# Optimization experiments

Measured on AMD Instinct MI355X. Metric: run time of the kernel, lower is better.

Reference implementation:

```python
import jax, jax.numpy as jnp
import numpy as np

N = 50000        # num nodes
NFEAT = 512      # input feature dim
NCLASS = 256     # output classes (out_features of out_att)
E_RAND = 800000  # random edges; + N self-loops
NEG_SLOPE = 0.2  # leakyrelu alpha


def setup_inputs() -> dict:
    key = jax.random.key(0)
    k1, k2, k3, k4 = jax.random.split(key, 4)
    x = jax.random.normal(k1, (N, NFEAT), dtype=jnp.float32)
    W = jax.random.normal(k2, (NFEAT, NCLASS), dtype=jnp.float32) / np.float32(np.sqrt(NFEAT))
    a = jax.random.normal(k3, (2 * NCLASS,), dtype=jnp.float32) / np.float32(np.sqrt(2 * NCLASS))
    rand_edges = jax.random.randint(k4, (2, E_RAND), 0, N, dtype=jnp.int32)
    self_loops = jnp.tile(jnp.arange(N, dtype=jnp.int32), (2, 1))
    edge_index = jnp.concatenate([rand_edges, self_loops], axis=1)  # [2, E]
    return {"x": x, "W": W, "a": a, "edge_index": edge_index}


def reference(x, W, a, edge_index):
    # Eval-mode SpGAT: dropout is identity (training=False).
    row, col = edge_index[0], edge_index[1]  # edge = adj.nonzero().t(): row aggregates from col
    h = x @ W                                # [N, F]
    F_out = h.shape[1]
    # a @ cat(h[row], h[col]) == (h @ a1)[row] + (h @ a2)[col]  (avoids [E, 2F] concat)
    s_row = h @ a[:F_out]                    # [N]
    s_col = h @ a[F_out:]                    # [N]
    logits = s_row[row] + s_col[col]         # [E]
    e = jnp.exp(-jax.nn.leaky_relu(logits, negative_slope=NEG_SLOPE))  # [E]
    rowsum = jax.ops.segment_sum(e, row, num_segments=N)               # [N]
    msgs = e[:, None] * h[col]                                         # [E, F]
    h_prime = jax.ops.segment_sum(msgs, row, num_segments=N) / rowsum[:, None]
    return jax.nn.log_softmax(jax.nn.elu(h_prime), axis=1)
```

## Files before the change

### kernel.cpp

```cpp
#include <hip/hip_runtime.h>
#include <math.h>

#define NNODES   50000
#define NFEAT    512
#define NCLASS   256
#define NEG_SLOPE 0.2f
#define MPAD     50048
#define GBLK     782
#define BCAP     64

typedef __attribute__((ext_vector_type(8))) short short8;
typedef __attribute__((ext_vector_type(4))) float floatx4;

__device__ __forceinline__ unsigned short f2bf(float f) {
    unsigned u = __builtin_bit_cast(unsigned, f);
    u += 0x7fffu + ((u >> 16) & 1u);
    return (unsigned short)(u >> 16);
}
__device__ __forceinline__ float bf2f_lo(unsigned u) {
    return __builtin_bit_cast(float, u << 16);
}
__device__ __forceinline__ float bf2f_hi(unsigned u) {
    return __builtin_bit_cast(float, u & 0xffff0000u);
}
__device__ __forceinline__ unsigned pack_bf16_rh(float lo, float hi) {
    const unsigned ulo = __builtin_bit_cast(unsigned, lo) + 0x8000u;
    const unsigned uhi = __builtin_bit_cast(unsigned, hi) + 0x8000u;
    return __builtin_amdgcn_perm(uhi, ulo, 0x07060302);
}

#if __has_builtin(__builtin_amdgcn_fdot2_f32_bf16)
#define HAVE_DOT2 1
typedef __attribute__((ext_vector_type(2))) __bf16 bfx2;
__device__ __forceinline__ float dot2bf(unsigned hpair, unsigned epair, float acc) {
    return __builtin_amdgcn_fdot2_f32_bf16(__builtin_bit_cast(bfx2, hpair),
                                           __builtin_bit_cast(bfx2, epair), acc, false);
}
#endif

__global__ __launch_bounds__(256) void init_kernel(const float* __restrict__ W,
                                                   unsigned short* __restrict__ Wt,
                                                   int* __restrict__ cursor, int zn) {
    const int i = blockIdx.x * 256 + threadIdx.x;
    const int n = i >> 9;
    const int k = i & 511;
    Wt[i] = f2bf(W[(size_t)k * NCLASS + n]);
    if (i < zn) cursor[i] = 0;
}

__global__ __launch_bounds__(256, 4) void gemm_mfma_kernel(const float* __restrict__ x,
                                                           const unsigned short* __restrict__ Wt,
                                                           unsigned short* __restrict__ hb,
                                                           const float* __restrict__ a,
                                                           float* __restrict__ s_row,
                                                           float* __restrict__ s_col,
                                                           int M) {
    __shared__ union {
        struct { short As[2][64 * 32]; short Bs[2][256 * 32]; } k;
        short Cs[32 * 260];
    } u;

    const int tid  = threadIdx.x;
    const int w    = tid >> 6;
    const int lane = tid & 63;
    const int rowbase = blockIdx.x * 64;

    const int wm = w & 1;
    const int wn = w >> 1;
    const int srow = lane >> 2;
    const int skq  = (lane & 3) << 3;
    const int fm = lane & 15;
    const int fq = lane >> 4;

    floatx4 acc[2][8];
#pragma unroll
    for (int i = 0; i < 2; ++i)
#pragma unroll
        for (int j = 0; j < 8; ++j)
            acc[i][j] = (floatx4){0.f, 0.f, 0.f, 0.f};

    const int arow = min(rowbase + w * 16 + srow, M - 1);
    const size_t abase = (size_t)arow * NFEAT + skq;
    const int lrowA = (w * 16 + srow) * 32 + skq;

#define STAGE_B(buf, k0)                                                                      \
    {                                                                                         \
        _Pragma("unroll")                                                                     \
        for (int t = 0; t < 4; ++t) {                                                         \
            const int seg = w * 4 + t;                                                        \
            const int nr  = seg * 16 + srow;                                                  \
            __builtin_amdgcn_global_load_lds(                                                 \
                (const __attribute__((address_space(1))) void*)(Wt + (size_t)nr * NFEAT + (k0) + skq), \
                (__attribute__((address_space(3))) void*)(&u.k.Bs[buf][seg * 512]), 16, 0, 0); \
        }                                                                                     \
    }

    STAGE_B(0, 0)
    {
        const float4* xp = (const float4*)&x[abase];
        const float4 u0 = xp[0];
        const float4 u1 = xp[1];
        uint4 o;
        o.x = pack_bf16_rh(u0.x, u0.y);
        o.y = pack_bf16_rh(u0.z, u0.w);
        o.z = pack_bf16_rh(u1.x, u1.y);
        o.w = pack_bf16_rh(u1.z, u1.w);
        *(uint4*)&u.k.As[0][lrowA] = o;
    }
    __syncthreads();

    int cur = 0;
    for (int k0 = 0; k0 < NFEAT; k0 += 32) {
        const int nxt = cur ^ 1;
        const bool have_next = (k0 + 32) < NFEAT;
        float4 p0, p1;
        if (have_next) {
            const float4* xp = (const float4*)&x[abase + k0 + 32];
            p0 = xp[0];
            p1 = xp[1];
            STAGE_B(nxt, k0 + 32)
        }

        short8 af[2];
#pragma unroll
        for (int mt = 0; mt < 2; ++mt)
            af[mt] = *(const short8*)&u.k.As[cur][(wm * 32 + mt * 16 + fm) * 32 + fq * 8];
#pragma unroll
        for (int nt = 0; nt < 8; ++nt) {
            const short8 bfr = *(const short8*)&u.k.Bs[cur][(wn * 128 + nt * 16 + fm) * 32 + fq * 8];
#pragma unroll
            for (int mt = 0; mt < 2; ++mt)
                acc[mt][nt] = __builtin_amdgcn_mfma_f32_16x16x32_bf16(af[mt], bfr, acc[mt][nt], 0, 0, 0);
        }

        if (have_next) {
            uint4 o;
            o.x = pack_bf16_rh(p0.x, p0.y);
            o.y = pack_bf16_rh(p0.z, p0.w);
            o.z = pack_bf16_rh(p1.x, p1.y);
            o.w = pack_bf16_rh(p1.z, p1.w);
            *(uint4*)&u.k.As[nxt][lrowA] = o;
        }
        __syncthreads();
        cur = nxt;
    }

#pragma unroll
    for (int p = 0; p < 2; ++p) {
        __syncthreads();
        if (wm == p) {
#pragma unroll
            for (int mt = 0; mt < 2; ++mt)
#pragma unroll
                for (int nt = 0; nt < 8; ++nt)
#pragma unroll
                    for (int r = 0; r < 4; ++r)
                        u.Cs[(mt * 16 + fq * 4 + r) * 260 + wn * 128 + nt * 16 + fm] =
                            (short)f2bf(acc[mt][nt][r]);
        }
        __syncthreads();
#pragma unroll
        for (int k = 0; k < 8; ++k) {
            const int idx = tid + k * 256;
            const int lrow = idx >> 6;
            const int c4 = (idx & 63) << 2;
            const int grow = rowbase + p * 32 + lrow;
            const uint2 vv = *(const uint2*)&u.Cs[lrow * 260 + c4];
            const float f0 = bf2f_lo(vv.x), f1 = bf2f_hi(vv.x);
            const float f2 = bf2f_lo(vv.y), f3 = bf2f_hi(vv.y);
            const float4 A1 = *(const float4*)&a[c4];
            const float4 A2 = *(const float4*)&a[NCLASS + c4];
            float p1 = f0 * A1.x + f1 * A1.y + f2 * A1.z + f3 * A1.w;
            float p2 = f0 * A2.x + f1 * A2.y + f2 * A2.z + f3 * A2.w;
#pragma unroll
            for (int off = 1; off < 64; off <<= 1) {
                p1 += __shfl_xor(p1, off);
                p2 += __shfl_xor(p2, off);
            }
            if (grow < M) {
                *(uint2*)&hb[(size_t)grow * NCLASS + c4] = vv;
                if (lane == 0) {
                    s_row[grow] = p1;
                    s_col[grow] = p2;
                }
            }
        }
    }
}

__global__ __launch_bounds__(256) void scatter_kernel(const int* __restrict__ row,
                                                      const int* __restrict__ col,
                                                      const float* __restrict__ s_row,
                                                      const float* __restrict__ s_col,
                                                      int* __restrict__ cursor,
                                                      int2* __restrict__ bucket, int e) {
    const int i = blockIdx.x * 256 + threadIdx.x;
    if (i >= e) return;
    const int r = row[i];
    const int c = col[i];
    const float logit = s_row[r] + s_col[c];
    const float lr = logit > 0.f ? logit : NEG_SLOPE * logit;
    const float ew = __expf(-lr);
    const int pos = atomicAdd(&cursor[r], 1);
    if (pos < BCAP) {
        int2 v;
        v.x = c;
        v.y = __builtin_bit_cast(int, ew);
        bucket[((size_t)r << 6) + pos] = v;
    }
}

__global__ __launch_bounds__(256) void aggregate_kernel(const unsigned short* __restrict__ hb,
                                                        const int2* __restrict__ bucket,
                                                        const int* __restrict__ cnt,
                                                        float* __restrict__ out, int n) {
    const int wave = (int)((blockIdx.x * (size_t)blockDim.x + threadIdx.x) >> 6);
    const int lane = threadIdx.x & 63;
    if (wave >= n) return;
    const int r = wave;
    const int jb = r << 6;
    const int je = jb + min(cnt[r], BCAP);
    const int fo = lane << 2;

    float rowsum = 0.f;
    int j = jb;

#ifdef HAVE_DOT2
    float ac0 = 0.f, ac1 = 0.f, ac2 = 0.f, ac3 = 0.f;
    for (; j + 3 < je; j += 4) {
        const int2 v0 = bucket[j];
        const int2 v1 = bucket[j + 1];
        const int2 v2 = bucket[j + 2];
        const int2 v3 = bucket[j + 3];
        const uint2 g0 = *(const uint2*)&hb[(size_t)v0.x * NCLASS + fo];
        const uint2 g1 = *(const uint2*)&hb[(size_t)v1.x * NCLASS + fo];
        const uint2 g2 = *(const uint2*)&hb[(size_t)v2.x * NCLASS + fo];
        const uint2 g3 = *(const uint2*)&hb[(size_t)v3.x * NCLASS + fo];
        const float e0 = __builtin_bit_cast(float, v0.y);
        const float e1 = __builtin_bit_cast(float, v1.y);
        const float e2 = __builtin_bit_cast(float, v2.y);
        const float e3 = __builtin_bit_cast(float, v3.y);
        const unsigned ep01 = pack_bf16_rh(e0, e1);
        const unsigned ep23 = pack_bf16_rh(e2, e3);
        rowsum += (e0 + e1) + (e2 + e3);
        ac0 = dot2bf(__builtin_amdgcn_perm(g1.x, g0.x, 0x05040100), ep01, ac0);
        ac1 = dot2bf(__builtin_amdgcn_perm(g1.x, g0.x, 0x07060302), ep01, ac1);
        ac2 = dot2bf(__builtin_amdgcn_perm(g1.y, g0.y, 0x05040100), ep01, ac2);
        ac3 = dot2bf(__builtin_amdgcn_perm(g1.y, g0.y, 0x07060302), ep01, ac3);
        ac0 = dot2bf(__builtin_amdgcn_perm(g3.x, g2.x, 0x05040100), ep23, ac0);
        ac1 = dot2bf(__builtin_amdgcn_perm(g3.x, g2.x, 0x07060302), ep23, ac1);
        ac2 = dot2bf(__builtin_amdgcn_perm(g3.y, g2.y, 0x05040100), ep23, ac2);
        ac3 = dot2bf(__builtin_amdgcn_perm(g3.y, g2.y, 0x07060302), ep23, ac3);
    }
    float4 acc = make_float4(ac0, ac1, ac2, ac3);
#else
    float4 acc = make_float4(0.f, 0.f, 0.f, 0.f);
    for (; j + 3 < je; j += 4) {
        const int2 v0 = bucket[j];
        const int2 v1 = bucket[j + 1];
        const int2 v2 = bucket[j + 2];
        const int2 v3 = bucket[j + 3];
        const uint2 g0 = *(const uint2*)&hb[(size_t)v0.x * NCLASS + fo];
        const uint2 g1 = *(const uint2*)&hb[(size_t)v1.x * NCLASS + fo];
        const uint2 g2 = *(const uint2*)&hb[(size_t)v2.x * NCLASS + fo];
        const uint2 g3 = *(const uint2*)&hb[(size_t)v3.x * NCLASS + fo];
        const float e0 = __builtin_bit_cast(float, v0.y);
        const float e1 = __builtin_bit_cast(float, v1.y);
        const float e2 = __builtin_bit_cast(float, v2.y);
        const float e3 = __builtin_bit_cast(float, v3.y);
        rowsum += (e0 + e1) + (e2 + e3);
        acc.x += e0 * bf2f_lo(g0.x) + e1 * bf2f_lo(g1.x) + e2 * bf2f_lo(g2.x) + e3 * bf2f_lo(g3.x);
        acc.y += e0 * bf2f_hi(g0.x) + e1 * bf2f_hi(g1.x) + e2 * bf2f_hi(g2.x) + e3 * bf2f_hi(g3.x);
        acc.z += e0 * bf2f_lo(g0.y) + e1 * bf2f_lo(g1.y) + e2 * bf2f_lo(g2.y) + e3 * bf2f_lo(g3.y);
        acc.w += e0 * bf2f_hi(g0.y) + e1 * bf2f_hi(g1.y) + e2 * bf2f_hi(g2.y) + e3 * bf2f_hi(g3.y);
    }
#endif
    for (; j < je; ++j) {
        const int2 v = bucket[j];
        const uint2 g = *(const uint2*)&hb[(size_t)v.x * NCLASS + fo];
        const float e = __builtin_bit_cast(float, v.y);
        rowsum += e;
        acc.x += e * bf2f_lo(g.x);
        acc.y += e * bf2f_hi(g.x);
        acc.z += e * bf2f_lo(g.y);
        acc.w += e * bf2f_hi(g.y);
    }

    const float inv = 1.f / rowsum;
    float v[4] = {acc.x * inv, acc.y * inv, acc.z * inv, acc.w * inv};
#pragma unroll
    for (int i = 0; i < 4; ++i)
        v[i] = v[i] > 0.f ? v[i] : __expf(v[i]) - 1.f;

    float m = fmaxf(fmaxf(v[0], v[1]), fmaxf(v[2], v[3]));
#pragma unroll
    for (int off = 32; off > 0; off >>= 1) m = fmaxf(m, __shfl_xor(m, off));
    float s = 0.f;
#pragma unroll
    for (int i = 0; i < 4; ++i) s += __expf(v[i] - m);
#pragma unroll
    for (int off = 32; off > 0; off >>= 1) s += __shfl_xor(s, off);
    const float lse = m + __logf(s);

    float4 o = make_float4(v[0] - lse, v[1] - lse, v[2] - lse, v[3] - lse);
    *(float4*)&out[(size_t)r * NCLASS + fo] = o;
}

extern "C" void kernel_launch(void* const* d_in, const int* in_sizes, int n_in,
                              void* d_out, int out_size, void* d_ws, size_t ws_size,
                              hipStream_t stream) {
    const float* x  = (const float*)d_in[0];
    const float* W  = (const float*)d_in[1];
    const float* a  = (const float*)d_in[2];
    const int* edge = (const int*)d_in[3];
    float* out = (float*)d_out;

    const int M = in_sizes[0] / NFEAT;
    const int E = in_sizes[3] / 2;
    const int* row = edge;
    const int* col = edge + E;

    char* ws = (char*)d_ws;
    size_t off = 0;
    auto carve = [&](size_t bytes) -> char* {
        char* p = ws + off;
        off = (off + bytes + 255) & ~(size_t)255;
        return p;
    };
    unsigned short* Wt = (unsigned short*)carve((size_t)NCLASS * NFEAT * sizeof(short));
    unsigned short* hb = (unsigned short*)carve((size_t)M * NCLASS * sizeof(short));
    int*   cursor   = (int*)carve((size_t)M * sizeof(int));
    float* s_row    = (float*)carve((size_t)M * sizeof(float));
    float* s_col    = (float*)carve((size_t)M * sizeof(float));
    int2*  bucket   = (int2*)carve((size_t)M * BCAP * sizeof(int2));

    init_kernel<<<512, 256, 0, stream>>>(W, Wt, cursor, M);

    gemm_mfma_kernel<<<GBLK, 256, 0, stream>>>(x, Wt, hb, a, s_row, s_col, M);

    scatter_kernel<<<(E + 255) / 256, 256, 0, stream>>>(row, col, s_row, s_col,
                                                        cursor, bucket, E);

    aggregate_kernel<<<(M + 3) / 4, 256, 0, stream>>>(hb, bucket, cursor, out, M);
}
```

Before: 305.6 us.

## Triple-buffer GEMM with direct fp32 LDS loads and defer edge weights to aggregation

The GEMM now streams fp32 x tiles and bf16 W tiles straight into LDS with async global_load_lds. It uses a three-stage ring with XOR-swizzled chunk placement and explicit vmcnt waits, and converts A to bf16 at fragment-read time instead of in registers before staging. This is meant to overlap global loads with MFMA work and cut register-staging overhead, at the cost of 72KB of LDS and a lower occupancy bound. Separately, the scatter kernel now stores only the column index. The attention weight is recomputed in the aggregation kernel from s_row/s_col, which halves the bucket traffic but adds a random s_col gather and an exp per edge there.

Measured after the change: 337.5 us. 1.1x slower.

```diff
diff --git a/kernel.cpp b/kernel.cpp
--- a/kernel.cpp
+++ b/kernel.cpp
@@ -5,7 +5,6 @@
 #define NFEAT    512
 #define NCLASS   256
 #define NEG_SLOPE 0.2f
-#define MPAD     50048
 #define GBLK     782
 #define BCAP     64
 
@@ -48,7 +47,7 @@
     if (i < zn) cursor[i] = 0;
 }
 
-__global__ __launch_bounds__(256, 4) void gemm_mfma_kernel(const float* __restrict__ x,
+__global__ __launch_bounds__(256, 2) void gemm_mfma_kernel(const float* __restrict__ x,
                                                            const unsigned short* __restrict__ Wt,
                                                            unsigned short* __restrict__ hb,
                                                            const float* __restrict__ a,
@@ -56,7 +55,7 @@
                                                            float* __restrict__ s_col,
                                                            int M) {
     __shared__ union {
-        struct { short As[2][64 * 32]; short Bs[2][256 * 32]; } k;
+        struct { float As[3][64 * 32]; short Bs[3][256 * 32]; } k;
         short Cs[32 * 260];
     } u;
 
@@ -67,8 +66,6 @@
 
     const int wm = w & 1;
     const int wn = w >> 1;
-    const int srow = lane >> 2;
-    const int skq  = (lane & 3) << 3;
     const int fm = lane & 15;
     const int fq = lane >> 4;
 
@@ -79,70 +76,92 @@
         for (int j = 0; j < 8; ++j)
             acc[i][j] = (floatx4){0.f, 0.f, 0.f, 0.f};
 
-    const int arow = min(rowbase + w * 16 + srow, M - 1);
-    const size_t abase = (size_t)arow * NFEAT + skq;
-    const int lrowA = (w * 16 + srow) * 32 + skq;
-
-#define STAGE_B(buf, k0)                                                                      \
+    const int arloc = lane >> 3;
+    const int alch  = (lane & 7) ^ arloc;
+    const int ar0 = min(rowbase + (w * 2 + 0) * 8 + arloc, M - 1);
+    const int ar1 = min(rowbase + (w * 2 + 1) * 8 + arloc, M - 1);
+    const float* asrc0 = x + (size_t)ar0 * NFEAT + alch * 4;
+    const float* asrc1 = x + (size_t)ar1 * NFEAT + alch * 4;
+    const int brloc = lane >> 2;
+    const int blch  = (lane & 3) ^ ((lane >> 3) & 3);
+    const unsigned short* bsrc[4];
+#pragma unroll
+    for (int t = 0; t < 4; ++t) {
+        const int seg = w * 4 + t;
+        bsrc[t] = Wt + (size_t)(seg * 16 + brloc) * NFEAT + blch * 8;
+    }
+
+#define STAGE_TILE(buf, k0)                                                                   \
     {                                                                                         \
+        __builtin_amdgcn_global_load_lds(                                                     \
+            (const __attribute__((address_space(1))) void*)(asrc0 + (k0)),                    \
+            (__attribute__((address_space(3))) void*)(&u.k.As[buf][(w * 2 + 0) * 8 * 32]),    \
+            16, 0, 0);                                                                        \
+        __builtin_amdgcn_global_load_lds(                                                     \
+            (const __attribute__((address_space(1))) void*)(asrc1 + (k0)),                    \
+            (__attribute__((address_space(3))) void*)(&u.k.As[buf][(w * 2 + 1) * 8 * 32]),    \
+            16, 0, 0);                                                                        \
         _Pragma("unroll")                                                                     \
         for (int t = 0; t < 4; ++t) {                                                         \
-            const int seg = w * 4 + t;                                                        \
-            const int nr  = seg * 16 + srow;                                                  \
             __builtin_amdgcn_global_load_lds(                                                 \
-                (const __attribute__((address_space(1))) void*)(Wt + (size_t)nr * NFEAT + (k0) + skq), \
-                (__attribute__((address_space(3))) void*)(&u.k.Bs[buf][seg * 512]), 16, 0, 0); \
+                (const __attribute__((address_space(1))) void*)(bsrc[t] + (k0)),              \
+                (__attribute__((address_space(3))) void*)(&u.k.Bs[buf][(w * 4 + t) * 512]),   \
+                16, 0, 0);                                                                    \
         }                                                                                     \
     }
 
-    STAGE_B(0, 0)
-    {
-        const float4* xp = (const float4*)&x[abase];
-        const float4 u0 = xp[0];
-        const float4 u1 = xp[1];
-        uint4 o;
-        o.x = pack_bf16_rh(u0.x, u0.y);
-        o.y = pack_bf16_rh(u0.z, u0.w);
-        o.z = pack_bf16_rh(u1.x, u1.y);
-        o.w = pack_bf16_rh(u1.z, u1.w);
-        *(uint4*)&u.k.As[0][lrowA] = o;
-    }
-    __syncthreads();
-
-    int cur = 0;
-    for (int k0 = 0; k0 < NFEAT; k0 += 32) {
-        const int nxt = cur ^ 1;
-        const bool have_next = (k0 + 32) < NFEAT;
-        float4 p0, p1;
-        if (have_next) {
-            const float4* xp = (const float4*)&x[abase + k0 + 32];
-            p0 = xp[0];
-            p1 = xp[1];
-            STAGE_B(nxt, k0 + 32)
+    STAGE_TILE(0, 0)
+    STAGE_TILE(1, 32)
+    asm volatile("s_waitcnt vmcnt(6)" ::: "memory");
+    __builtin_amdgcn_sched_barrier(0);
+    __builtin_amdgcn_s_barrier();
+    __builtin_amdgcn_sched_barrier(0);
+
+    const int keyB = (fm >> 1) & 3;
+    const int r7   = fm & 7;
+
+#pragma unroll
+    for (int k = 0; k < 16; ++k) {
+        const int cur = k % 3;
+        if (k < 14) {
+            const int nb = (k + 2) % 3;
+            STAGE_TILE(nb, (k + 2) * 32)
         }
 
         short8 af[2];
 #pragma unroll
-        for (int mt = 0; mt < 2; ++mt)
-            af[mt] = *(const short8*)&u.k.As[cur][(wm * 32 + mt * 16 + fm) * 32 + fq * 8];
+        for (int mt = 0; mt < 2; ++mt) {
+            const int row = wm * 32 + mt * 16 + fm;
+            const int p0 = (2 * fq) ^ r7;
+            const int p1 = (2 * fq + 1) ^ r7;
+            const float4 a0 = *(const float4*)&u.k.As[cur][row * 32 + p0 * 4];
+            const float4 a1 = *(const float4*)&u.k.As[cur][row * 32 + p1 * 4];
+            uint4 o;
+            o.x = pack_bf16_rh(a0.x, a0.y);
+            o.y = pack_bf16_rh(a0.z, a0.w);
+            o.z = pack_bf16_rh(a1.x, a1.y);
+            o.w = pack_bf16_rh(a1.z, a1.w);
+            af[mt] = __builtin_bit_cast(short8, o);
+        }
 #pragma unroll
         for (int nt = 0; nt < 8; ++nt) {
-            const short8 bfr = *(const short8*)&u.k.Bs[cur][(wn * 128 + nt * 16 + fm) * 32 + fq * 8];
-#pragma unroll
-            for (int mt = 0; mt < 2; ++mt)
-                acc[mt][nt] = __builtin_amdgcn_mfma_f32_16x16x32_bf16(af[mt], bfr, acc[mt][nt], 0, 0, 0);
-        }
-
-        if (have_next) {
-            uint4 o;
-            o.x = pack_bf16_rh(p0.x, p0.y);
-            o.y = pack_bf16_rh(p0.z, p0.w);
-            o.z = pack_bf16_rh(p1.x, p1.y);
-            o.w = pack_bf16_rh(p1.z, p1.w);
-            *(uint4*)&u.k.As[nxt][lrowA] = o;
-        }
-        __syncthreads();
-        cur = nxt;
+            const int row = wn * 128 + nt * 16 + fm;
+            const int pb = fq ^ keyB;
+            const short8 bfr = *(const short8*)&u.k.Bs[cur][row * 32 + pb * 8];
+            acc[0][nt] = __builtin_amdgcn_mfma_f32_16x16x32_bf16(af[0], bfr, acc[0][nt], 0, 0, 0);
+            acc[1][nt] = __builtin_amdgcn_mfma_f32_16x16x32_bf16(af[1], bfr, acc[1][nt], 0, 0, 0);
+        }
+
+        if (k < 15) {
+            if (k < 14) {
+                asm volatile("s_waitcnt vmcnt(6)" ::: "memory");
+            } else {
+                asm volatile("s_waitcnt vmcnt(0)" ::: "memory");
+            }
+            __builtin_amdgcn_sched_barrier(0);
+            __builtin_amdgcn_s_barrier();
+            __builtin_amdgcn_sched_barrier(0);
+        }
     }
 
 #pragma unroll
@@ -160,8 +179,8 @@
         }
         __syncthreads();
 #pragma unroll
-        for (int k = 0; k < 8; ++k) {
-            const int idx = tid + k * 256;
+        for (int kk = 0; kk < 8; ++kk) {
+            const int idx = tid + kk * 256;
             const int lrow = idx >> 6;
             const int c4 = (idx & 63) << 2;
             const int grow = rowbase + p * 32 + lrow;
@@ -190,29 +209,21 @@
 
 __global__ __launch_bounds__(256) void scatter_kernel(const int* __restrict__ row,
                                                       const int* __restrict__ col,
-                                                      const float* __restrict__ s_row,
-                                                      const float* __restrict__ s_col,
                                                       int* __restrict__ cursor,
-                                                      int2* __restrict__ bucket, int e) {
+                                                      int* __restrict__ bucket, int e) {
     const int i = blockIdx.x * 256 + threadIdx.x;
     if (i >= e) return;
     const int r = row[i];
     const int c = col[i];
-    const float logit = s_row[r] + s_col[c];
-    const float lr = logit > 0.f ? logit : NEG_SLOPE * logit;
-    const float ew = __expf(-lr);
     const int pos = atomicAdd(&cursor[r], 1);
-    if (pos < BCAP) {
-        int2 v;
-        v.x = c;
-        v.y = __builtin_bit_cast(int, ew);
-        bucket[((size_t)r << 6) + pos] = v;
-    }
+    if (pos < BCAP) bucket[((size_t)r << 6) + pos] = c;
 }
 
 __global__ __launch_bounds__(256) void aggregate_kernel(const unsigned short* __restrict__ hb,
-                                                        const int2* __restrict__ bucket,
+                                                        const int* __restrict__ bucket,
                                                         const int* __restrict__ cnt,
+                                                        const float* __restrict__ s_row,
+                                                        const float* __restrict__ s_col,
                                                         float* __restrict__ out, int n) {
     const int wave = (int)((blockIdx.x * (size_t)blockDim.x + threadIdx.x) >> 6);
     const int lane = threadIdx.x & 63;
@@ -221,25 +232,27 @@
     const int jb = r << 6;
     const int je = jb + min(cnt[r], BCAP);
     const int fo = lane << 2;
+    const float sr = s_row[r];
 
     float rowsum = 0.f;
     int j = jb;
+
+#define EDGE_E(c) ({ const float _l = sr + s_col[c];                         \
+                     const float _lr = _l > 0.f ? _l : NEG_SLOPE * _l;       \
+                     __expf(-_lr); })
 
 #ifdef HAVE_DOT2
     float ac0 = 0.f, ac1 = 0.f, ac2 = 0.f, ac3 = 0.f;
     for (; j + 3 < je; j += 4) {
-        const int2 v0 = bucket[j];
-        const int2 v1 = bucket[j + 1];
-        const int2 v2 = bucket[j + 2];
-        const int2 v3 = bucket[j + 3];
-        const uint2 g0 = *(const uint2*)&hb[(size_t)v0.x * NCLASS + fo];
-        const uint2 g1 = *(const uint2*)&hb[(size_t)v1.x * NCLASS + fo];
-        const uint2 g2 = *(const uint2*)&hb[(size_t)v2.x * NCLASS + fo];
-        const uint2 g3 = *(const uint2*)&hb[(size_t)v3.x * NCLASS + fo];
-        const float e0 = __builtin_bit_cast(float, v0.y);
-        const float e1 = __builtin_bit_cast(float, v1.y);
-        const float e2 = __builtin_bit_cast(float, v2.y);
-        const float e3 = __builtin_bit_cast(float, v3.y);
+        const int4 cv = *(const int4*)&bucket[j];
+        const uint2 g0 = *(const uint2*)&hb[(size_t)cv.x * NCLASS + fo];
+        const uint2 g1 = *(const uint2*)&hb[(size_t)cv.y * NCLASS + fo];
+        const uint2 g2 = *(const uint2*)&hb[(size_t)cv.z * NCLASS + fo];
+        const uint2 g3 = *(const uint2*)&hb[(size_t)cv.w * NCLASS + fo];
+        const float e0 = EDGE_E(cv.x);
+        const float e1 = EDGE_E(cv.y);
+        const float e2 = EDGE_E(cv.z);
+        const float e3 = EDGE_E(cv.w);
         const unsigned ep01 = pack_bf16_rh(e0, e1);
         const unsigned ep23 = pack_bf16_rh(e2, e3);
         rowsum += (e0 + e1) + (e2 + e3);
@@ -256,18 +269,15 @@
 #else
     float4 acc = make_float4(0.f, 0.f, 0.f, 0.f);
     for (; j + 3 < je; j += 4) {
-        const int2 v0 = bucket[j];
-        const int2 v1 = bucket[j + 1];
-        const int2 v2 = bucket[j + 2];
-        const int2 v3 = bucket[j + 3];
-        const uint2 g0 = *(const uint2*)&hb[(size_t)v0.x * NCLASS + fo];
-        const uint2 g1 = *(const uint2*)&hb[(size_t)v1.x * NCLASS + fo];
-        const uint2 g2 = *(const uint2*)&hb[(size_t)v2.x * NCLASS + fo];
-        const uint2 g3 = *(const uint2*)&hb[(size_t)v3.x * NCLASS + fo];
-        const float e0 = __builtin_bit_cast(float, v0.y);
-        const float e1 = __builtin_bit_cast(float, v1.y);
-        const float e2 = __builtin_bit_cast(float, v2.y);
-        const float e3 = __builtin_bit_cast(float, v3.y);
+        const int4 cv = *(const int4*)&bucket[j];
+        const uint2 g0 = *(const uint2*)&hb[(size_t)cv.x * NCLASS + fo];
+        const uint2 g1 = *(const uint2*)&hb[(size_t)cv.y * NCLASS + fo];
+        const uint2 g2 = *(const uint2*)&hb[(size_t)cv.z * NCLASS + fo];
+        const uint2 g3 = *(const uint2*)&hb[(size_t)cv.w * NCLASS + fo];
+        const float e0 = EDGE_E(cv.x);
+        const float e1 = EDGE_E(cv.y);
+        const float e2 = EDGE_E(cv.z);
+        const float e3 = EDGE_E(cv.w);
         rowsum += (e0 + e1) + (e2 + e3);
         acc.x += e0 * bf2f_lo(g0.x) + e1 * bf2f_lo(g1.x) + e2 * bf2f_lo(g2.x) + e3 * bf2f_lo(g3.x);
         acc.y += e0 * bf2f_hi(g0.x) + e1 * bf2f_hi(g1.x) + e2 * bf2f_hi(g2.x) + e3 * bf2f_hi(g3.x);
@@ -276,9 +286,9 @@
     }
 #endif
     for (; j < je; ++j) {
-        const int2 v = bucket[j];
-        const uint2 g = *(const uint2*)&hb[(size_t)v.x * NCLASS + fo];
-        const float e = __builtin_bit_cast(float, v.y);
+        const int c = bucket[j];
+        const uint2 g = *(const uint2*)&hb[(size_t)c * NCLASS + fo];
+        const float e = EDGE_E(c);
         rowsum += e;
         acc.x += e * bf2f_lo(g.x);
         acc.y += e * bf2f_hi(g.x);
@@ -332,14 +342,13 @@
     int*   cursor   = (int*)carve((size_t)M * sizeof(int));
     float* s_row    = (float*)carve((size_t)M * sizeof(float));
     float* s_col    = (float*)carve((size_t)M * sizeof(float));
-    int2*  bucket   = (int2*)carve((size_t)M * BCAP * sizeof(int2));
+    int*   bucket   = (int*)carve((size_t)M * BCAP * sizeof(int));
 
     init_kernel<<<512, 256, 0, stream>>>(W, Wt, cursor, M);
 
     gemm_mfma_kernel<<<GBLK, 256, 0, stream>>>(x, Wt, hb, a, s_row, s_col, M);
 
-    scatter_kernel<<<(E + 255) / 256, 256, 0, stream>>>(row, col, s_row, s_col,
-                                                        cursor, bucket, E);
-
-    aggregate_kernel<<<(M + 3) / 4, 256, 0, stream>>>(hb, bucket, cursor, out, M);
-}
+    scatter_kernel<<<(E + 255) / 256, 256, 0, stream>>>(row, col, cursor, bucket, E);
+
+    aggregate_kernel<<<(M + 3) / 4, 256, 0, stream>>>(hb, bucket, cursor, s_row, s_col, out, M);
+}
```

## Fuse edge bucketing into GEMM tail and compute edge weights in aggregation

Applied to the files above, without the earlier changes.

Removes the separate scatter kernel. Edge bucketing now runs as a grid-stride loop at the end of the GEMM kernel and stores only column indices, halving the bucket size. Edge weights are recomputed in the aggregation kernel from s_row/s_col, trading an extra random s_col gather and exp per edge for one fewer launch and less bucket traffic. The atomics inside the GEMM kernel add to its tail time but remove one launch and its s_row/s_col dependency.

New measurement: 314.9 us. +3.0%, slower.

```diff
diff --git a/kernel.cpp b/kernel.cpp
--- a/kernel.cpp
+++ b/kernel.cpp
@@ -5,7 +5,6 @@
 #define NFEAT    512
 #define NCLASS   256
 #define NEG_SLOPE 0.2f
-#define MPAD     50048
 #define GBLK     782
 #define BCAP     64
 
@@ -54,7 +53,11 @@
                                                            const float* __restrict__ a,
                                                            float* __restrict__ s_row,
                                                            float* __restrict__ s_col,
-                                                           int M) {
+                                                           const int* __restrict__ erow,
+                                                           const int* __restrict__ ecol,
+                                                           int* __restrict__ cursor,
+                                                           int* __restrict__ bucket,
+                                                           int M, int E) {
     __shared__ union {
         struct { short As[2][64 * 32]; short Bs[2][256 * 32]; } k;
         short Cs[32 * 260];
@@ -128,9 +131,8 @@
 #pragma unroll
         for (int nt = 0; nt < 8; ++nt) {
             const short8 bfr = *(const short8*)&u.k.Bs[cur][(wn * 128 + nt * 16 + fm) * 32 + fq * 8];
-#pragma unroll
-            for (int mt = 0; mt < 2; ++mt)
-                acc[mt][nt] = __builtin_amdgcn_mfma_f32_16x16x32_bf16(af[mt], bfr, acc[mt][nt], 0, 0, 0);
+            acc[0][nt] = __builtin_amdgcn_mfma_f32_16x16x32_bf16(af[0], bfr, acc[0][nt], 0, 0, 0);
+            acc[1][nt] = __builtin_amdgcn_mfma_f32_16x16x32_bf16(af[1], bfr, acc[1][nt], 0, 0, 0);
         }
 
         if (have_next) {
@@ -160,8 +162,8 @@
         }
         __syncthreads();
 #pragma unroll
-        for (int k = 0; k < 8; ++k) {
-            const int idx = tid + k * 256;
+        for (int kk = 0; kk < 8; ++kk) {
+            const int idx = tid + kk * 256;
             const int lrow = idx >> 6;
             const int c4 = (idx & 63) << 2;
             const int grow = rowbase + p * 32 + lrow;
@@ -186,33 +188,21 @@
             }
         }
     }
-}
-
-__global__ __launch_bounds__(256) void scatter_kernel(const int* __restrict__ row,
-                                                      const int* __restrict__ col,
-                                                      const float* __restrict__ s_row,
-                                                      const float* __restrict__ s_col,
-                                                      int* __restrict__ cursor,
-                                                      int2* __restrict__ bucket, int e) {
-    const int i = blockIdx.x * 256 + threadIdx.x;
-    if (i >= e) return;
-    const int r = row[i];
-    const int c = col[i];
-    const float logit = s_row[r] + s_col[c];
-    const float lr = logit > 0.f ? logit : NEG_SLOPE * logit;
-    const float ew = __expf(-lr);
-    const int pos = atomicAdd(&cursor[r], 1);
-    if (pos < BCAP) {
-        int2 v;
-        v.x = c;
-        v.y = __builtin_bit_cast(int, ew);
-        bucket[((size_t)r << 6) + pos] = v;
+
+    const int gtid = blockIdx.x * 256 + tid;
+    for (int i = gtid; i < E; i += GBLK * 256) {
+        const int r = erow[i];
+        const int c = ecol[i];
+        const int pos = atomicAdd(&cursor[r], 1);
+        if (pos < BCAP) bucket[((size_t)r << 6) + pos] = c;
     }
 }
 
 __global__ __launch_bounds__(256) void aggregate_kernel(const unsigned short* __restrict__ hb,
-                                                        const int2* __restrict__ bucket,
+                                                        const int* __restrict__ bucket,
                                                         const int* __restrict__ cnt,
+                                                        const float* __restrict__ s_row,
+                                                        const float* __restrict__ s_col,
                                                         float* __restrict__ out, int n) {
     const int wave = (int)((blockIdx.x * (size_t)blockDim.x + threadIdx.x) >> 6);
     const int lane = threadIdx.x & 63;
@@ -221,25 +211,27 @@
     const int jb = r << 6;
     const int je = jb + min(cnt[r], BCAP);
     const int fo = lane << 2;
+    const float sr = s_row[r];
 
     float rowsum = 0.f;
     int j = jb;
+
+#define EDGE_E(c) ({ const float _l = sr + s_col[c];                         \
+                     const float _lr = _l > 0.f ? _l : NEG_SLOPE * _l;       \
+                     __expf(-_lr); })
 
 #ifdef HAVE_DOT2
     float ac0 = 0.f, ac1 = 0.f, ac2 = 0.f, ac3 = 0.f;
     for (; j + 3 < je; j += 4) {
-        const int2 v0 = bucket[j];
-        const int2 v1 = bucket[j + 1];
-        const int2 v2 = bucket[j + 2];
-        const int2 v3 = bucket[j + 3];
-        const uint2 g0 = *(const uint2*)&hb[(size_t)v0.x * NCLASS + fo];
-        const uint2 g1 = *(const uint2*)&hb[(size_t)v1.x * NCLASS + fo];
-        const uint2 g2 = *(const uint2*)&hb[(size_t)v2.x * NCLASS + fo];
-        const uint2 g3 = *(const uint2*)&hb[(size_t)v3.x * NCLASS + fo];
-        const float e0 = __builtin_bit_cast(float, v0.y);
-        const float e1 = __builtin_bit_cast(float, v1.y);
-        const float e2 = __builtin_bit_cast(float, v2.y);
-        const float e3 = __builtin_bit_cast(float, v3.y);
+        const int4 cv = *(const int4*)&bucket[j];
+        const uint2 g0 = *(const uint2*)&hb[(size_t)cv.x * NCLASS + fo];
+        const uint2 g1 = *(const uint2*)&hb[(size_t)cv.y * NCLASS + fo];
+        const uint2 g2 = *(const uint2*)&hb[(size_t)cv.z * NCLASS + fo];
+        const uint2 g3 = *(const uint2*)&hb[(size_t)cv.w * NCLASS + fo];
+        const float e0 = EDGE_E(cv.x);
+        const float e1 = EDGE_E(cv.y);
+        const float e2 = EDGE_E(cv.z);
+        const float e3 = EDGE_E(cv.w);
         const unsigned ep01 = pack_bf16_rh(e0, e1);
         const unsigned ep23 = pack_bf16_rh(e2, e3);
         rowsum += (e0 + e1) + (e2 + e3);
@@ -256,18 +248,15 @@
 #else
     float4 acc = make_float4(0.f, 0.f, 0.f, 0.f);
     for (; j + 3 < je; j += 4) {
-        const int2 v0 = bucket[j];
-        const int2 v1 = bucket[j + 1];
-        const int2 v2 = bucket[j + 2];
-        const int2 v3 = bucket[j + 3];
-        const uint2 g0 = *(const uint2*)&hb[(size_t)v0.x * NCLASS + fo];
-        const uint2 g1 = *(const uint2*)&hb[(size_t)v1.x * NCLASS + fo];
-        const uint2 g2 = *(const uint2*)&hb[(size_t)v2.x * NCLASS + fo];
-        const uint2 g3 = *(const uint2*)&hb[(size_t)v3.x * NCLASS + fo];
-        const float e0 = __builtin_bit_cast(float, v0.y);
-        const float e1 = __builtin_bit_cast(float, v1.y);
-        const float e2 = __builtin_bit_cast(float, v2.y);
-        const float e3 = __builtin_bit_cast(float, v3.y);
+        const int4 cv = *(const int4*)&bucket[j];
+        const uint2 g0 = *(const uint2*)&hb[(size_t)cv.x * NCLASS + fo];
+        const uint2 g1 = *(const uint2*)&hb[(size_t)cv.y * NCLASS + fo];
+        const uint2 g2 = *(const uint2*)&hb[(size_t)cv.z * NCLASS + fo];
+        const uint2 g3 = *(const uint2*)&hb[(size_t)cv.w * NCLASS + fo];
+        const float e0 = EDGE_E(cv.x);
+        const float e1 = EDGE_E(cv.y);
+        const float e2 = EDGE_E(cv.z);
+        const float e3 = EDGE_E(cv.w);
         rowsum += (e0 + e1) + (e2 + e3);
         acc.x += e0 * bf2f_lo(g0.x) + e1 * bf2f_lo(g1.x) + e2 * bf2f_lo(g2.x) + e3 * bf2f_lo(g3.x);
         acc.y += e0 * bf2f_hi(g0.x) + e1 * bf2f_hi(g1.x) + e2 * bf2f_hi(g2.x) + e3 * bf2f_hi(g3.x);
@@ -276,9 +265,9 @@
     }
 #endif
     for (; j < je; ++j) {
-        const int2 v = bucket[j];
-        const uint2 g = *(const uint2*)&hb[(size_t)v.x * NCLASS + fo];
-        const float e = __builtin_bit_cast(float, v.y);
+        const int c = bucket[j];
+        const uint2 g = *(const uint2*)&hb[(size_t)c * NCLASS + fo];
+        const float e = EDGE_E(c);
         rowsum += e;
         acc.x += e * bf2f_lo(g.x);
         acc.y += e * bf2f_hi(g.x);
@@ -332,14 +321,12 @@
     int*   cursor   = (int*)carve((size_t)M * sizeof(int));
     float* s_row    = (float*)carve((size_t)M * sizeof(float));
     float* s_col    = (float*)carve((size_t)M * sizeof(float));
-    int2*  bucket   = (int2*)carve((size_t)M * BCAP * sizeof(int2));
+    int*   bucket   = (int*)carve((size_t)M * BCAP * sizeof(int));
 
     init_kernel<<<512, 256, 0, stream>>>(W, Wt, cursor, M);
 
-    gemm_mfma_kernel<<<GBLK, 256, 0, stream>>>(x, Wt, hb, a, s_row, s_col, M);
-
-    scatter_kernel<<<(E + 255) / 256, 256, 0, stream>>>(row, col, s_row, s_col,
-                                                        cursor, bucket, E);
-
-    aggregate_kernel<<<(M + 3) / 4, 256, 0, stream>>>(hb, bucket, cursor, out, M);
-}
+    gemm_mfma_kernel<<<GBLK, 256, 0, stream>>>(x, Wt, hb, a, s_row, s_col,
+                                               row, col, cursor, bucket, M, E);
+
+    aggregate_kernel<<<(M + 3) / 4, 256, 0, stream>>>(hb, bucket, cursor, s_row, s_col, out, M);
+}
```
